# Kernel optimization log

Hardware: AMD Instinct MI355X
Metric: run time of the kernel (lower is better)

## Reference

```python
import jax, jax.numpy as jnp
import numpy as np
import math

B, H, N = 16, 768, 2048  # batch, hidden_size, num_patches


def setup_inputs() -> dict:
    key = jax.random.key(0)
    k1, k2, k3, k4 = jax.random.split(key, 4)
    shape = (B, H, N)
    return {
        "query": jax.random.normal(k1, shape, dtype=jnp.float32),
        "key": jax.random.normal(k2, shape, dtype=jnp.float32),
        "value": jax.random.normal(k3, shape, dtype=jnp.float32),
        "key_pe": jax.random.normal(k4, shape, dtype=jnp.float32),
    }


def reference(query, key, value, key_pe):
    # query/key/value/key_pe: [B, H, N]
    hidden_size = query.shape[1]
    scale = 1.0 / math.sqrt(hidden_size)
    # content + positional scores: [B, N, N]  (q^T k + q^T pe)
    attn = jnp.einsum('bhn,bhm->bnm', query, key) \
         + jnp.einsum('bhn,bhm->bnm', query, key_pe)
    attn = jax.nn.softmax(attn * scale, axis=-1)
    # combine with values: [B, N, N] x [B, N, H] -> [B, N, H] -> [B, H, N]
    out = jnp.einsum('bnm,bhm->bhn', attn, value)
    return out
```

## Files before the change

### kernel.cpp

```cpp
#include <hip/hip_runtime.h>

#define B_ 16
#define H_ 768
#define N_ 2048
#define SCALE 0.03608439182435161f

typedef unsigned short u16;
typedef unsigned int u32;
typedef __attribute__((ext_vector_type(8))) short short8;
typedef __attribute__((ext_vector_type(4))) float float4v;

__device__ __forceinline__ u16 f2bf(float f) {
  u32 u = __float_as_uint(f);
  u32 r = (u + 0x7FFFu + ((u >> 16) & 1u)) >> 16;
  return (u16)r;
}
__device__ __forceinline__ float bf2f(u16 h) { return __uint_as_float(((u32)h) << 16); }
__device__ __forceinline__ u32 pk2(float a, float b) {
  return (u32)f2bf(a) | ((u32)f2bf(b) << 16);
}

__device__ __forceinline__ void dma16(const void* g, void* l) {
  __builtin_amdgcn_global_load_lds(
      (const __attribute__((address_space(1))) void*)g,
      (__attribute__((address_space(3))) void*)l, 16, 0, 0);
}

__global__ __launch_bounds__(256) void kt_transpose(
    const float* __restrict__ q, const float* __restrict__ k,
    const float* __restrict__ pe, u16* __restrict__ qT, u16* __restrict__ keffT) {
  __shared__ float tile[64][65];
  const int t = threadIdx.x;
  const int b = blockIdx.z & 15;
  const int which = blockIdx.z >> 4;
  const float* src = which ? k : q;
  u16* dst = which ? keffT : qT;
  const size_t inb = (size_t)b * H_ * N_;
  const size_t outb = (size_t)b * N_ * H_;
  const int n0 = blockIdx.x * 64;
  const int h0 = blockIdx.y * 64;
  const int col4 = (t & 15) * 4;
  const int r0 = t >> 4;
#pragma unroll
  for (int i = 0; i < 4; ++i) {
    const int row = r0 + i * 16;
    const size_t idx = inb + (size_t)(h0 + row) * N_ + (n0 + col4);
    float4 v = *(const float4*)&src[idx];
    if (which) {
      float4 p = *(const float4*)&pe[idx];
      v.x += p.x; v.y += p.y; v.z += p.z; v.w += p.w;
    }
    tile[row][col4 + 0] = v.x;
    tile[row][col4 + 1] = v.y;
    tile[row][col4 + 2] = v.z;
    tile[row][col4 + 3] = v.w;
  }
  __syncthreads();
  const int w2 = t & 15;
  const int r1 = t >> 4;
#pragma unroll
  for (int i = 0; i < 4; ++i) {
    const int row = r1 + i * 16;
    uint2 u;
    u.x = pk2(tile[4 * w2 + 0][row], tile[4 * w2 + 1][row]);
    u.y = pk2(tile[4 * w2 + 2][row], tile[4 * w2 + 3][row]);
    *(uint2*)(dst + outb + (size_t)(n0 + row) * H_ + (h0 + 4 * w2)) = u;
  }
}

__global__ __launch_bounds__(256) void kv_convert(
    const float* __restrict__ v, u16* __restrict__ vB) {
  const size_t i = ((size_t)blockIdx.x * 256 + threadIdx.x) * 8;
  float4 a = *(const float4*)&v[i];
  float4 b = *(const float4*)&v[i + 4];
  uint4 o;
  o.x = pk2(a.x, a.y);
  o.y = pk2(a.z, a.w);
  o.z = pk2(b.x, b.y);
  o.w = pk2(b.z, b.w);
  *(uint4*)&vB[i] = o;
}

__global__ __launch_bounds__(512, 2) void k1_qk_gemm(
    const u16* __restrict__ qT, const u16* __restrict__ keffT, u16* __restrict__ S) {
  __shared__ __align__(16) u16 lds[2][2][256 * 64];
  const int t = threadIdx.x;
  const int lane = t & 63;
  const int wv = t >> 6;
  const int wm = wv >> 2;
  const int wn = wv & 3;
  const int b = blockIdx.z;
  const int m0 = blockIdx.x * 256;
  const int n0 = blockIdx.y * 256;
  const u16* Ab = qT + (size_t)b * N_ * H_ + (size_t)n0 * H_;
  const u16* Bb = keffT + (size_t)b * N_ * H_ + (size_t)m0 * H_;
  float4v acc[8][4] = {};
  const int fr = lane & 15;
  const int fk = (lane >> 4) * 8;

#define STAGE_K1(buf, kt)                                                     \
  {                                                                           \
    const int kbase = (kt)*64;                                                \
    _Pragma("unroll") for (int r = 0; r < 4; ++r) {                           \
      const int c = r * 512 + t;                                              \
      const int row = c >> 3;                                                 \
      const int k8 = (c & 7) * 8;                                             \
      dma16(Ab + (size_t)row * H_ + (kbase + k8), &lds[buf][0][c * 8]);       \
      dma16(Bb + (size_t)row * H_ + (kbase + k8), &lds[buf][1][c * 8]);       \
    }                                                                         \
  }

  STAGE_K1(0, 0);
  __syncthreads();
  const int NT = H_ / 64;
  for (int kt = 0; kt < NT; ++kt) {
    const int buf = kt & 1;
    if (kt + 1 < NT) STAGE_K1(buf ^ 1, kt + 1);
    const u16* LA = &lds[buf][0][0];
    const u16* LB = &lds[buf][1][0];
#pragma unroll
    for (int ks = 0; ks < 2; ++ks) {
      short8 af[8], bfv[4];
#pragma unroll
      for (int i = 0; i < 8; ++i)
        af[i] = *(const short8*)&LA[(wm * 128 + i * 16 + fr) * 64 + ks * 32 + fk];
#pragma unroll
      for (int j = 0; j < 4; ++j)
        bfv[j] = *(const short8*)&LB[(wn * 64 + j * 16 + fr) * 64 + ks * 32 + fk];
#pragma unroll
      for (int i = 0; i < 8; ++i)
#pragma unroll
        for (int j = 0; j < 4; ++j)
          acc[i][j] = __builtin_amdgcn_mfma_f32_16x16x32_bf16(af[i], bfv[j], acc[i][j], 0, 0, 0);
    }
    __syncthreads();
  }
#undef STAGE_K1

  float* ldsC = (float*)&lds[0][0][0];
  const int cr = lane >> 4, cc = lane & 15;
  const size_t Sb = (size_t)b * N_ * N_;
  const int orow = t >> 3;
  const int ocol = (t & 7) * 32;
  for (int ch = 0; ch < 4; ++ch) {
    if (wm == (ch >> 1)) {
#pragma unroll
      for (int ii = 0; ii < 4; ++ii) {
        const int i = (ch & 1) * 4 + ii;
#pragma unroll
        for (int j = 0; j < 4; ++j)
#pragma unroll
          for (int r = 0; r < 4; ++r)
            ldsC[(ii * 16 + cr * 4 + r) * 264 + (wn * 64 + j * 16 + cc)] = acc[i][j][r];
      }
    }
    __syncthreads();
    const float* srcp = &ldsC[orow * 264 + ocol];
    uint4 o4[4];
#pragma unroll
    for (int e = 0; e < 4; ++e) {
      float4 f0 = *(const float4*)&srcp[e * 8];
      float4 f1 = *(const float4*)&srcp[e * 8 + 4];
      o4[e].x = pk2(f0.x, f0.y);
      o4[e].y = pk2(f0.z, f0.w);
      o4[e].z = pk2(f1.x, f1.y);
      o4[e].w = pk2(f1.z, f1.w);
    }
    u16* dst = S + Sb + (size_t)(n0 + ch * 64 + orow) * N_ + (m0 + ocol);
#pragma unroll
    for (int e = 0; e < 4; ++e) *(uint4*)(dst + e * 8) = o4[e];
    __syncthreads();
  }
}

__global__ __launch_bounds__(256) void k1b_softmax(u16* __restrict__ S) {
  const int t = threadIdx.x;
  const int lane = t & 63;
  const int wv = t >> 6;
  const size_t row = (size_t)blockIdx.x * 4 + wv;
  u16* base = S + row * N_;
  float x[32];
#pragma unroll
  for (int c = 0; c < 4; ++c) {
    uint4 u = *(const uint4*)&base[c * 512 + lane * 8];
    const u32 uu[4] = {u.x, u.y, u.z, u.w};
#pragma unroll
    for (int e = 0; e < 4; ++e) {
      x[c * 8 + e * 2] = bf2f((u16)(uu[e] & 0xFFFFu));
      x[c * 8 + e * 2 + 1] = bf2f((u16)(uu[e] >> 16));
    }
  }
  float mx = -1e30f;
#pragma unroll
  for (int e = 0; e < 32; ++e) mx = fmaxf(mx, x[e]);
#pragma unroll
  for (int off = 32; off > 0; off >>= 1) mx = fmaxf(mx, __shfl_xor(mx, off));
  float sum = 0.f;
#pragma unroll
  for (int e = 0; e < 32; ++e) {
    x[e] = __expf((x[e] - mx) * SCALE);
    sum += x[e];
  }
#pragma unroll
  for (int off = 32; off > 0; off >>= 1) sum += __shfl_xor(sum, off);
  const float rinv = 1.0f / sum;
#pragma unroll
  for (int c = 0; c < 4; ++c) {
    uint4 o;
    o.x = pk2(x[c * 8 + 0] * rinv, x[c * 8 + 1] * rinv);
    o.y = pk2(x[c * 8 + 2] * rinv, x[c * 8 + 3] * rinv);
    o.z = pk2(x[c * 8 + 4] * rinv, x[c * 8 + 5] * rinv);
    o.w = pk2(x[c * 8 + 6] * rinv, x[c * 8 + 7] * rinv);
    *(uint4*)&base[c * 512 + lane * 8] = o;
  }
}

__global__ __launch_bounds__(256) void k2_pv_gemm(
    const u16* __restrict__ vB, const u16* __restrict__ P, float* __restrict__ out) {
  __shared__ __align__(16) u16 ldsA[128 * 32];
  __shared__ __align__(16) u16 ldsB[128 * 32];
  const int t = threadIdx.x;
  const int lane = t & 63;
  const int wv = t >> 6;
  const int wr = wv >> 1, wc = wv & 1;
  const int b = blockIdx.z;
  const int n0 = blockIdx.x * 128;
  const int h0 = blockIdx.y * 128;
  const u16* Ab = vB + (size_t)b * H_ * N_ + (size_t)h0 * N_;
  const u16* Bb = P + (size_t)b * N_ * N_ + (size_t)n0 * N_;
  float4v acc[4][4] = {};
  const int fr = lane & 15;
  const int fk = (lane >> 4) * 8;
  for (int k0 = 0; k0 < N_; k0 += 32) {
    __syncthreads();
#pragma unroll
    for (int r = 0; r < 2; ++r) {
      const int c = r * 256 + t;
      const int row = c >> 2;
      const int co = (c & 3) * 8;
      dma16(Ab + (size_t)row * N_ + (k0 + co), &ldsA[c * 8]);
      dma16(Bb + (size_t)row * N_ + (k0 + co), &ldsB[c * 8]);
    }
    __syncthreads();
    short8 af[4], bfv[4];
#pragma unroll
    for (int i = 0; i < 4; ++i)
      af[i] = *(const short8*)&ldsA[(wr * 64 + i * 16 + fr) * 32 + fk];
#pragma unroll
    for (int j = 0; j < 4; ++j)
      bfv[j] = *(const short8*)&ldsB[(wc * 64 + j * 16 + fr) * 32 + fk];
#pragma unroll
    for (int i = 0; i < 4; ++i)
#pragma unroll
      for (int j = 0; j < 4; ++j)
        acc[i][j] = __builtin_amdgcn_mfma_f32_16x16x32_bf16(af[i], bfv[j], acc[i][j], 0, 0, 0);
  }
  const int cr = lane >> 4, cc = lane & 15;
  const size_t ob = (size_t)b * H_ * N_;
#pragma unroll
  for (int i = 0; i < 4; ++i) {
    const int hh = h0 + wr * 64 + i * 16 + cr * 4;
#pragma unroll
    for (int j = 0; j < 4; ++j) {
      const int nn = n0 + wc * 64 + j * 16 + cc;
#pragma unroll
      for (int r = 0; r < 4; ++r)
        out[ob + (size_t)(hh + r) * N_ + nn] = acc[i][j][r];
    }
  }
}

extern "C" void kernel_launch(void* const* d_in, const int* in_sizes, int n_in,
                              void* d_out, int out_size, void* d_ws, size_t ws_size,
                              hipStream_t stream) {
  const float* q = (const float*)d_in[0];
  const float* k = (const float*)d_in[1];
  const float* v = (const float*)d_in[2];
  const float* pe = (const float*)d_in[3];
  float* out = (float*)d_out;
  char* ws = (char*)d_ws;
  u16* qT = (u16*)ws;
  u16* keffT = (u16*)(ws + 50331648);
  u16* S = (u16*)(ws + 100663296);
  u16* vB = (u16*)ws;

  hipLaunchKernelGGL(kt_transpose, dim3(32, 12, 32), dim3(256), 0, stream, q, k, pe, qT, keffT);
  hipLaunchKernelGGL(k1_qk_gemm, dim3(8, 8, 16), dim3(512), 0, stream, qT, keffT, S);
  hipLaunchKernelGGL(kv_convert, dim3(12288), dim3(256), 0, stream, v, vB);
  hipLaunchKernelGGL(k1b_softmax, dim3(8192), dim3(256), 0, stream, S);
  hipLaunchKernelGGL(k2_pv_gemm, dim3(16, 6, 16), dim3(256), 0, stream, vB, S, out);
}
```

Before: 728.0 us.

## Triple-buffer GEMM LDS pipelines with XOR swizzle, block remap, and hardware bf16 pack

Both GEMM kernels now use a three-stage LDS ring with K=32 slices. Waits use explicit vmcnt counts, so two tiles stay in flight while the current one is computed. LDS rows are stored with an XOR swizzle to avoid bank conflicts on fragment reads. Block IDs are remapped so consecutive workgroups share operands across XCDs. The PV GEMM grows to 256-wide tiles with 512 threads, and the software bf16 rounding is replaced by the v_cvt_pk_bf16_f32 instruction. The risks are correctness of the hand-tuned waitcnt values and register pressure from the larger PV tile.

```diff
diff --git a/kernel.cpp b/kernel.cpp
--- a/kernel.cpp
+++ b/kernel.cpp
@@ -10,14 +10,11 @@
 typedef __attribute__((ext_vector_type(8))) short short8;
 typedef __attribute__((ext_vector_type(4))) float float4v;
 
-__device__ __forceinline__ u16 f2bf(float f) {
-  u32 u = __float_as_uint(f);
-  u32 r = (u + 0x7FFFu + ((u >> 16) & 1u)) >> 16;
-  return (u16)r;
-}
 __device__ __forceinline__ float bf2f(u16 h) { return __uint_as_float(((u32)h) << 16); }
 __device__ __forceinline__ u32 pk2(float a, float b) {
-  return (u32)f2bf(a) | ((u32)f2bf(b) << 16);
+  u32 r;
+  asm("v_cvt_pk_bf16_f32 %0, %1, %2" : "=v"(r) : "v"(a), "v"(b));
+  return r;
 }
 
 __device__ __forceinline__ void dma16(const void* g, void* l) {
@@ -81,65 +78,79 @@
   *(uint4*)&vB[i] = o;
 }
 
+#define K1_LOADS 4
 __global__ __launch_bounds__(512, 2) void k1_qk_gemm(
     const u16* __restrict__ qT, const u16* __restrict__ keffT, u16* __restrict__ S) {
-  __shared__ __align__(16) u16 lds[2][2][256 * 64];
+  __shared__ __align__(16) u16 lds[3][2][256 * 32];
   const int t = threadIdx.x;
   const int lane = t & 63;
   const int wv = t >> 6;
   const int wm = wv >> 2;
   const int wn = wv & 3;
-  const int b = blockIdx.z;
-  const int m0 = blockIdx.x * 256;
-  const int n0 = blockIdx.y * 256;
-  const u16* Ab = qT + (size_t)b * N_ * H_ + (size_t)n0 * H_;
-  const u16* Bb = keffT + (size_t)b * N_ * H_ + (size_t)m0 * H_;
+  int lid = blockIdx.x + (blockIdx.y << 3) + (blockIdx.z << 6);
+  lid = (lid & 7) * 128 + (lid >> 3);
+  const int bx = lid & 7;
+  const int by = (lid >> 3) & 7;
+  const int bz = lid >> 6;
+  const int m0 = bx * 256;
+  const int n0 = by * 256;
+  const u16* Ab = qT + (size_t)bz * N_ * H_ + (size_t)n0 * H_;
+  const u16* Bb = keffT + (size_t)bz * N_ * H_ + (size_t)m0 * H_;
   float4v acc[8][4] = {};
   const int fr = lane & 15;
-  const int fk = (lane >> 4) * 8;
-
-#define STAGE_K1(buf, kt)                                                     \
+  const int g = lane >> 4;
+
+#define STAGE1(buf, kt_)                                                      \
   {                                                                           \
-    const int kbase = (kt)*64;                                                \
-    _Pragma("unroll") for (int r = 0; r < 4; ++r) {                           \
+    const int kb = (kt_) * 32;                                                \
+    _Pragma("unroll") for (int r = 0; r < 2; ++r) {                           \
       const int c = r * 512 + t;                                              \
-      const int row = c >> 3;                                                 \
-      const int k8 = (c & 7) * 8;                                             \
-      dma16(Ab + (size_t)row * H_ + (kbase + k8), &lds[buf][0][c * 8]);       \
-      dma16(Bb + (size_t)row * H_ + (kbase + k8), &lds[buf][1][c * 8]);       \
+      const int row = c >> 2;                                                 \
+      const int sl = c & 3;                                                   \
+      const int gcol = kb + ((sl ^ ((row >> 1) & 3)) << 3);                   \
+      dma16(Ab + (size_t)row * H_ + gcol, &lds[buf][0][c * 8]);               \
+      dma16(Bb + (size_t)row * H_ + gcol, &lds[buf][1][c * 8]);               \
     }                                                                         \
   }
 
-  STAGE_K1(0, 0);
-  __syncthreads();
-  const int NT = H_ / 64;
-  for (int kt = 0; kt < NT; ++kt) {
-    const int buf = kt & 1;
-    if (kt + 1 < NT) STAGE_K1(buf ^ 1, kt + 1);
-    const u16* LA = &lds[buf][0][0];
-    const u16* LB = &lds[buf][1][0];
-#pragma unroll
-    for (int ks = 0; ks < 2; ++ks) {
-      short8 af[8], bfv[4];
-#pragma unroll
-      for (int i = 0; i < 8; ++i)
-        af[i] = *(const short8*)&LA[(wm * 128 + i * 16 + fr) * 64 + ks * 32 + fk];
+  STAGE1(0, 0);
+  STAGE1(1, 1);
+  asm volatile("s_waitcnt vmcnt(%0)" ::"i"(K1_LOADS) : "memory");
+  __builtin_amdgcn_s_barrier();
+  const int NT = H_ / 32;
+  for (int kt_ = 0; kt_ < NT; ++kt_) {
+    const int b = kt_ % 3;
+    const bool pf = (kt_ + 2 < NT);
+    if (pf) STAGE1((kt_ + 2) % 3, kt_ + 2);
+    const u16* LA = &lds[b][0][0];
+    const u16* LB = &lds[b][1][0];
+    short8 bfv[4], af[8];
+#pragma unroll
+    for (int j = 0; j < 4; ++j) {
+      const int row = wn * 64 + j * 16 + fr;
+      bfv[j] = *(const short8*)&LB[row * 32 + ((g ^ ((row >> 1) & 3)) << 3)];
+    }
+#pragma unroll
+    for (int i = 0; i < 8; ++i) {
+      const int row = wm * 128 + i * 16 + fr;
+      af[i] = *(const short8*)&LA[row * 32 + ((g ^ ((row >> 1) & 3)) << 3)];
+    }
+#pragma unroll
+    for (int i = 0; i < 8; ++i)
 #pragma unroll
       for (int j = 0; j < 4; ++j)
-        bfv[j] = *(const short8*)&LB[(wn * 64 + j * 16 + fr) * 64 + ks * 32 + fk];
-#pragma unroll
-      for (int i = 0; i < 8; ++i)
-#pragma unroll
-        for (int j = 0; j < 4; ++j)
-          acc[i][j] = __builtin_amdgcn_mfma_f32_16x16x32_bf16(af[i], bfv[j], acc[i][j], 0, 0, 0);
-    }
-    __syncthreads();
-  }
-#undef STAGE_K1
+        acc[i][j] = __builtin_amdgcn_mfma_f32_16x16x32_bf16(af[i], bfv[j], acc[i][j], 0, 0, 0);
+    if (pf)
+      asm volatile("s_waitcnt vmcnt(%0) lgkmcnt(0)" ::"i"(K1_LOADS) : "memory");
+    else
+      asm volatile("s_waitcnt vmcnt(0) lgkmcnt(0)" ::: "memory");
+    __builtin_amdgcn_s_barrier();
+  }
+#undef STAGE1
 
   float* ldsC = (float*)&lds[0][0][0];
   const int cr = lane >> 4, cc = lane & 15;
-  const size_t Sb = (size_t)b * N_ * N_;
+  const size_t Sb = (size_t)bz * N_ * N_;
   const int orow = t >> 3;
   const int ocol = (t & 7) * 32;
   for (int ch = 0; ch < 4; ++ch) {
@@ -215,54 +226,88 @@
   }
 }
 
-__global__ __launch_bounds__(256) void k2_pv_gemm(
+#define K2_LOADS 3
+__global__ __launch_bounds__(512, 2) void k2_pv_gemm(
     const u16* __restrict__ vB, const u16* __restrict__ P, float* __restrict__ out) {
-  __shared__ __align__(16) u16 ldsA[128 * 32];
-  __shared__ __align__(16) u16 ldsB[128 * 32];
+  __shared__ __align__(16) u16 lds[3][12288];
   const int t = threadIdx.x;
   const int lane = t & 63;
   const int wv = t >> 6;
-  const int wr = wv >> 1, wc = wv & 1;
-  const int b = blockIdx.z;
-  const int n0 = blockIdx.x * 128;
-  const int h0 = blockIdx.y * 128;
-  const u16* Ab = vB + (size_t)b * H_ * N_ + (size_t)h0 * N_;
-  const u16* Bb = P + (size_t)b * N_ * N_ + (size_t)n0 * N_;
+  const int wm = wv >> 2;
+  const int wn = wv & 3;
+  int lid = blockIdx.x + 8 * (blockIdx.y + 6 * blockIdx.z);
+  lid = (lid & 7) * 96 + (lid >> 3);
+  const int bx = lid & 7;
+  const int rem = lid >> 3;
+  const int by = rem % 6;
+  const int bz = rem / 6;
+  const int n0 = bx * 256;
+  const int h0 = by * 128;
+  const u16* Ab = vB + (size_t)bz * H_ * N_ + (size_t)h0 * N_;
+  const u16* Bb = P + (size_t)bz * N_ * N_ + (size_t)n0 * N_;
   float4v acc[4][4] = {};
   const int fr = lane & 15;
-  const int fk = (lane >> 4) * 8;
-  for (int k0 = 0; k0 < N_; k0 += 32) {
-    __syncthreads();
-#pragma unroll
-    for (int r = 0; r < 2; ++r) {
-      const int c = r * 256 + t;
-      const int row = c >> 2;
-      const int co = (c & 3) * 8;
-      dma16(Ab + (size_t)row * N_ + (k0 + co), &ldsA[c * 8]);
-      dma16(Bb + (size_t)row * N_ + (k0 + co), &ldsB[c * 8]);
-    }
-    __syncthreads();
+  const int g = lane >> 4;
+
+#define STAGE2(buf, kt_)                                                      \
+  {                                                                           \
+    const int kb = (kt_) * 32;                                                \
+    {                                                                         \
+      const int row = t >> 2, sl = t & 3;                                     \
+      const int gcol = kb + ((sl ^ ((row >> 1) & 3)) << 3);                   \
+      dma16(Ab + (size_t)row * N_ + gcol, &lds[buf][t * 8]);                  \
+    }                                                                         \
+    _Pragma("unroll") for (int r = 0; r < 2; ++r) {                           \
+      const int c = r * 512 + t;                                              \
+      const int row = c >> 2, sl = c & 3;                                     \
+      const int gcol = kb + ((sl ^ ((row >> 1) & 3)) << 3);                   \
+      dma16(Bb + (size_t)row * N_ + gcol, &lds[buf][4096 + c * 8]);           \
+    }                                                                         \
+  }
+
+  STAGE2(0, 0);
+  STAGE2(1, 1);
+  asm volatile("s_waitcnt vmcnt(%0)" ::"i"(K2_LOADS) : "memory");
+  __builtin_amdgcn_s_barrier();
+  const int NT = N_ / 32;
+  for (int kt_ = 0; kt_ < NT; ++kt_) {
+    const int b = kt_ % 3;
+    const bool pf = (kt_ + 2 < NT);
+    if (pf) STAGE2((kt_ + 2) % 3, kt_ + 2);
+    const u16* LA = &lds[b][0];
+    const u16* LB = &lds[b][4096];
     short8 af[4], bfv[4];
 #pragma unroll
-    for (int i = 0; i < 4; ++i)
-      af[i] = *(const short8*)&ldsA[(wr * 64 + i * 16 + fr) * 32 + fk];
-#pragma unroll
-    for (int j = 0; j < 4; ++j)
-      bfv[j] = *(const short8*)&ldsB[(wc * 64 + j * 16 + fr) * 32 + fk];
+    for (int i = 0; i < 4; ++i) {
+      const int row = wm * 64 + i * 16 + fr;
+      af[i] = *(const short8*)&LA[row * 32 + ((g ^ ((row >> 1) & 3)) << 3)];
+    }
+#pragma unroll
+    for (int j = 0; j < 4; ++j) {
+      const int row = wn * 64 + j * 16 + fr;
+      bfv[j] = *(const short8*)&LB[row * 32 + ((g ^ ((row >> 1) & 3)) << 3)];
+    }
 #pragma unroll
     for (int i = 0; i < 4; ++i)
 #pragma unroll
       for (int j = 0; j < 4; ++j)
         acc[i][j] = __builtin_amdgcn_mfma_f32_16x16x32_bf16(af[i], bfv[j], acc[i][j], 0, 0, 0);
-  }
+    if (pf)
+      asm volatile("s_waitcnt vmcnt(%0) lgkmcnt(0)" ::"i"(K2_LOADS) : "memory");
+    else
+      asm volatile("s_waitcnt vmcnt(0) lgkmcnt(0)" ::: "memory");
+    __builtin_amdgcn_s_barrier();
+  }
+#undef STAGE2
+
   const int cr = lane >> 4, cc = lane & 15;
-  const size_t ob = (size_t)b * H_ * N_;
+  const size_t ob = (size_t)bz * H_ * N_;
 #pragma unroll
   for (int i = 0; i < 4; ++i) {
-    const int hh = h0 + wr * 64 + i * 16 + cr * 4;
+    const int hh = h0 + wm * 64 + i * 16 + cr * 4;
 #pragma unroll
     for (int j = 0; j < 4; ++j) {
-      const int nn = n0 + wc * 64 + j * 16 + cc;
+      const int nn = n0 + wn * 64 + j * 16 + cc;
 #pragma unroll
       for (int r = 0; r < 4; ++r)
         out[ob + (size_t)(hh + r) * N_ + nn] = acc[i][j][r];
@@ -288,5 +333,5 @@
   hipLaunchKernelGGL(k1_qk_gemm, dim3(8, 8, 16), dim3(512), 0, stream, qT, keffT, S);
   hipLaunchKernelGGL(kv_convert, dim3(12288), dim3(256), 0, stream, v, vB);
   hipLaunchKernelGGL(k1b_softmax, dim3(8192), dim3(256), 0, stream, S);
-  hipLaunchKernelGGL(k2_pv_gemm, dim3(16, 6, 16), dim3(256), 0, stream, vB, S, out);
-}
+  hipLaunchKernelGGL(k2_pv_gemm, dim3(8, 6, 16), dim3(512), 0, stream, vB, S, out);
+}
```

After: 673.4 us. 7.5% less time.
